# Kernel tuning notes

Measured on AMD Instinct MI355X. Metric: run time of the kernel, lower is better.

Reference implementation:

```python
import jax, jax.numpy as jnp
import numpy as np

D_MODEL = 2048
NUM_HEADS = 16
HEAD_DIM = D_MODEL // NUM_HEADS  # 128


def setup_inputs() -> dict:
    key = jax.random.key(0)
    ks = jax.random.split(key, 11)
    B, S = 2, 2048
    s = 0.02
    return {
        "q": jax.random.normal(ks[0], (B, S, D_MODEL), jnp.float32),
        "k": jax.random.normal(ks[1], (B, S, D_MODEL), jnp.float32),
        "v": jax.random.normal(ks[2], (B, S, D_MODEL), jnp.float32),
        "Wq": jax.random.normal(ks[3], (D_MODEL, D_MODEL), jnp.float32) * s,
        "bq": jnp.zeros((D_MODEL,), jnp.float32),
        "Wk": jax.random.normal(ks[4], (D_MODEL, HEAD_DIM), jnp.float32) * s,
        "bk": jnp.zeros((HEAD_DIM,), jnp.float32),
        "Wv": jax.random.normal(ks[5], (D_MODEL, HEAD_DIM), jnp.float32) * s,
        "bv": jnp.zeros((HEAD_DIM,), jnp.float32),
        "Wo": jax.random.normal(ks[6], (D_MODEL, D_MODEL), jnp.float32) * s,
        "bo": jnp.zeros((D_MODEL,), jnp.float32),
    }


def reference(q, k, v, Wq, bq, Wk, bk, Wv, bv, Wo, bo):
    B, Sq, _ = q.shape
    Skv = k.shape[1]
    # Query projection -> per-head queries [B, H, Sq, Dh]
    qh = (q @ Wq + bq).reshape(B, Sq, NUM_HEADS, HEAD_DIM).transpose(0, 2, 1, 3)
    # Shared single-head K/V projections [B, Skv, Dh]
    kh = k @ Wk + bk
    vh = v @ Wv + bv
    scale = 1.0 / jnp.sqrt(jnp.asarray(HEAD_DIM, qh.dtype))
    # MQA: broadcast shared K over heads without materializing per-head copies
    scores = jnp.einsum("bhqd,bkd->bhqk", qh, kh) * scale  # [B, H, Sq, Skv]
    attn = jax.nn.softmax(scores, axis=-1)
    out = jnp.einsum("bhqk,bkd->bhqd", attn, vh)  # [B, H, Sq, Dh]
    out = out.transpose(0, 2, 1, 3).reshape(B, Sq, D_MODEL)
    return out @ Wo + bo
```

## Files before the change

kernel.cpp:

```cpp
#include <hip/hip_runtime.h>

typedef unsigned short u16;
typedef unsigned int u32;
typedef __bf16 bf16_t;
typedef __attribute__((ext_vector_type(8))) bf16_t bf16x8;
typedef __attribute__((ext_vector_type(4))) float f32x4;

__device__ inline u16 f2bf(float f) {
    union { float f; u32 u; } v; v.f = f;
    u32 u = v.u;
    u32 r = (u + 0x7fffu + ((u >> 16) & 1u)) >> 16;
    return (u16)r;
}

__device__ inline void async_cp16(const void* g, void* l) {
    __builtin_amdgcn_global_load_lds((const __attribute__((address_space(1))) void*)g,
                                     (__attribute__((address_space(3))) void*)l, 16, 0, 0);
}

__global__ __launch_bounds__(256) void cvt3(const float* __restrict__ a,
                                            const float* __restrict__ b,
                                            const float* __restrict__ c,
                                            u16* __restrict__ oa, u16* __restrict__ ob,
                                            u16* __restrict__ oc) {
    int z = blockIdx.y;
    const float* in = z == 0 ? a : (z == 1 ? b : c);
    u16* out = z == 0 ? oa : (z == 1 ? ob : oc);
    int i = (blockIdx.x * 256 + threadIdx.x) * 4;
    float4 f = *(const float4*)(in + i);
    ushort4 o;
    o.x = f2bf(f.x); o.y = f2bf(f.y); o.z = f2bf(f.z); o.w = f2bf(f.w);
    *(ushort4*)(out + i) = o;
}

__global__ __launch_bounds__(256) void transpose2(const float* __restrict__ W0,
                                                  u16* __restrict__ T0,
                                                  const float* __restrict__ W1,
                                                  u16* __restrict__ T1,
                                                  int K, int N) {
    const float* W = blockIdx.z == 0 ? W0 : W1;
    u16* WT = blockIdx.z == 0 ? T0 : T1;
    __shared__ float tile[32][33];
    int tr0 = blockIdx.x * 32;
    int tc0 = blockIdx.y * 32;
    int t = threadIdx.x;
    for (int i = 0; i < 4; i++) {
        int idx = t + i * 256; int r = idx >> 5, c = idx & 31;
        tile[r][c] = W[(size_t)(tr0 + r) * N + tc0 + c];
    }
    __syncthreads();
    for (int i = 0; i < 4; i++) {
        int idx = t + i * 256; int r = idx >> 5, c = idx & 31;
        WT[(size_t)(tc0 + r) * K + tr0 + c] = f2bf(tile[c][r]);
    }
}

template <typename OUT_T>
__global__ __launch_bounds__(256) void gemm_bt(const u16* __restrict__ A,
                                               const u16* __restrict__ BT,
                                               const float* __restrict__ bias,
                                               OUT_T* __restrict__ C,
                                               int M, int N, int K, int ldout) {
    __shared__ u16 sA[128 * 32];
    __shared__ u16 sB[128 * 32];
    int t = threadIdx.x, lane = t & 63, wv = t >> 6;
    int quad = lane >> 4, c16 = lane & 15;
    int bm = blockIdx.x * 128, bn = blockIdx.y * 128;
    int wm = (wv & 1) * 64, wn = (wv >> 1) * 64;
    f32x4 acc[4][4] = {};

    int srow = wv * 32 + (lane >> 2);
    int scol = (lane & 3) * 8;
    const u16* Ag = A + (size_t)(bm + srow) * K + scol;
    const u16* Bg = BT + (size_t)(bn + srow) * K + scol;
    u16* sAd = &sA[(wv * 32) * 32];
    u16* sBd = &sB[(wv * 32) * 32];

    for (int k0 = 0; k0 < K; k0 += 32) {
        __syncthreads();
        async_cp16(Ag + k0, sAd);
        async_cp16(Ag + (size_t)16 * K + k0, sAd + 16 * 32);
        async_cp16(Bg + k0, sBd);
        async_cp16(Bg + (size_t)16 * K + k0, sBd + 16 * 32);
        __syncthreads();
        bf16x8 af[4], bfr[4];
        for (int mi = 0; mi < 4; mi++)
            af[mi] = *(const bf16x8*)&sA[(wm + mi * 16 + c16) * 32 + quad * 8];
        for (int ni = 0; ni < 4; ni++)
            bfr[ni] = *(const bf16x8*)&sB[(wn + ni * 16 + c16) * 32 + quad * 8];
        for (int mi = 0; mi < 4; mi++)
            for (int ni = 0; ni < 4; ni++)
                acc[mi][ni] = __builtin_amdgcn_mfma_f32_16x16x32_bf16(
                    af[mi], bfr[ni], acc[mi][ni], 0, 0, 0);
    }

    for (int mi = 0; mi < 4; mi++) {
        for (int ni = 0; ni < 4; ni++) {
            int col = bn + wn + ni * 16 + c16;
            float bv = bias[col];
            for (int p = 0; p < 4; p++) {
                int row = bm + wm + mi * 16 + quad * 4 + p;
                float v = acc[mi][ni][p] + bv;
                size_t off = (size_t)row * ldout + col;
                if constexpr (__is_same(OUT_T, u16)) C[off] = f2bf(v);
                else C[off] = v;
            }
        }
    }
}

__global__ __launch_bounds__(256) void gemm_kv_sk(const u16* __restrict__ kbf,
                                                  const u16* __restrict__ vbf,
                                                  const u16* __restrict__ WkT,
                                                  const u16* __restrict__ WvT,
                                                  float* __restrict__ kacc,
                                                  float* __restrict__ vacc,
                                                  int K, int KS) {
    bool isv = blockIdx.y == 1;
    const u16* A = isv ? vbf : kbf;
    const u16* BT = isv ? WvT : WkT;
    float* aco = isv ? vacc : kacc;
    __shared__ u16 sA[128 * 32];
    __shared__ u16 sB[128 * 32];
    int t = threadIdx.x, lane = t & 63, wv = t >> 6;
    int quad = lane >> 4, c16 = lane & 15;
    int bm = blockIdx.x * 128;
    int wm = (wv & 1) * 64, wn = (wv >> 1) * 64;
    f32x4 acc[4][4] = {};

    int srow = wv * 32 + (lane >> 2);
    int scol = (lane & 3) * 8;
    const u16* Ag = A + (size_t)(bm + srow) * K + scol;
    const u16* Bg = BT + (size_t)srow * K + scol;
    u16* sAd = &sA[(wv * 32) * 32];
    u16* sBd = &sB[(wv * 32) * 32];

    int kbeg = blockIdx.z * KS;
    for (int k0 = kbeg; k0 < kbeg + KS; k0 += 32) {
        __syncthreads();
        async_cp16(Ag + k0, sAd);
        async_cp16(Ag + (size_t)16 * K + k0, sAd + 16 * 32);
        async_cp16(Bg + k0, sBd);
        async_cp16(Bg + (size_t)16 * K + k0, sBd + 16 * 32);
        __syncthreads();
        bf16x8 af[4], bfr[4];
        for (int mi = 0; mi < 4; mi++)
            af[mi] = *(const bf16x8*)&sA[(wm + mi * 16 + c16) * 32 + quad * 8];
        for (int ni = 0; ni < 4; ni++)
            bfr[ni] = *(const bf16x8*)&sB[(wn + ni * 16 + c16) * 32 + quad * 8];
        for (int mi = 0; mi < 4; mi++)
            for (int ni = 0; ni < 4; ni++)
                acc[mi][ni] = __builtin_amdgcn_mfma_f32_16x16x32_bf16(
                    af[mi], bfr[ni], acc[mi][ni], 0, 0, 0);
    }

    for (int mi = 0; mi < 4; mi++)
        for (int ni = 0; ni < 4; ni++) {
            int col = wn + ni * 16 + c16;
            for (int p = 0; p < 4; p++) {
                int row = bm + wm + mi * 16 + quad * 4 + p;
                atomicAdd(&aco[(size_t)row * 128 + col], acc[mi][ni][p]);
            }
        }
}

__global__ __launch_bounds__(256) void cvt_kv(const float* __restrict__ kacc,
                                              const float* __restrict__ vacc,
                                              const float* __restrict__ bk,
                                              const float* __restrict__ bv,
                                              u16* __restrict__ khb,
                                              u16* __restrict__ vhT,
                                              int M) {
    int t = threadIdx.x;
    int tr0 = blockIdx.x * 32;
    int tc0 = blockIdx.y * 32;
    if (blockIdx.z == 0) {
        for (int i = 0; i < 4; i++) {
            int idx = t + i * 256; int r = idx >> 5, c = idx & 31;
            khb[(size_t)(tr0 + r) * 128 + tc0 + c] =
                f2bf(kacc[(size_t)(tr0 + r) * 128 + tc0 + c] + bk[tc0 + c]);
        }
    } else {
        __shared__ float tile[32][33];
        for (int i = 0; i < 4; i++) {
            int idx = t + i * 256; int r = idx >> 5, c = idx & 31;
            tile[r][c] = vacc[(size_t)(tr0 + r) * 128 + tc0 + c] + bv[tc0 + c];
        }
        __syncthreads();
        for (int i = 0; i < 4; i++) {
            int idx = t + i * 256; int r = idx >> 5, c = idx & 31;
            vhT[(size_t)(tc0 + r) * M + tr0 + c] = f2bf(tile[c][r]);
        }
    }
}

__global__ __launch_bounds__(256, 2) void mqa_attn(const u16* __restrict__ qh,
                                                   const u16* __restrict__ kh,
                                                   const u16* __restrict__ vhT,
                                                   u16* __restrict__ outp,
                                                   int S) {
    constexpr float CEXP = 0.08838834764831845f * 1.4426950408889634f;
    __shared__ u16 smem[40960];
    u16* sK0 = smem;
    u16* sV0 = smem + 16384;
    u16* sP  = smem + 32768;

    int t = threadIdx.x, lane = t & 63, wv = t >> 6;
    int quad = lane >> 4, c16 = lane & 15;
    int rx = c16 & 7;
    int b = blockIdx.z, h = blockIdx.y;
    int q0w = blockIdx.x * 128 + wv * 32;
    int BS = b * S;

    bf16x8 aq[2][4];
    for (int mi = 0; mi < 2; mi++) {
        const u16* qp = qh + (size_t)(BS + q0w + mi * 16 + c16) * 2048 + h * 128 + quad * 8;
        for (int c = 0; c < 4; c++) aq[mi][c] = *(const bf16x8*)(qp + c * 32);
    }

    f32x4 out[2][8] = {};
    f32x4 lsumv[2] = {};
    u16* sPw = sP + wv * 2048;

    int ksub = lane >> 4, kch = lane & 15;
    int klx = (wv * 4 + ksub) & 7;
    const u16* kgb = kh + (size_t)(BS + wv * 4 + ksub) * 128 + ((kch ^ klx) * 8);
    int vsub = lane >> 3, vch = lane & 7;
    int vlx = vsub & 7;
    const u16* vgb = vhT + (size_t)(wv * 8 + vsub) * 4096 + BS + ((vch ^ vlx) * 8);

    u16* kb0 = sK0 + (wv * 4) * 128;
    u16* vb0 = sV0 + (wv * 8) * 64;

    auto STAGE = [&](int kv0, int d) {
        u16* kb = kb0 + d * 8192;
        u16* vb = vb0 + d * 8192;
        for (int p = 0; p < 4; p++)
            async_cp16(kgb + (size_t)(kv0 + p * 16) * 128, kb + p * 2048);
        for (int p = 0; p < 4; p++)
            async_cp16(vgb + (size_t)(p * 32) * 4096 + kv0, vb + p * 2048);
    };

    const int NT = S >> 6;
    STAGE(0, 0);
    __syncthreads();

    for (int tt = 0; tt < NT; tt++) {
        int cur = tt & 1;
        if (tt + 1 < NT) STAGE((tt + 1) * 64, cur ^ 1);
        const u16* sKc = sK0 + cur * 8192;
        const u16* sVc = sV0 + cur * 8192;

        for (int ni = 0; ni < 4; ni++) {
            f32x4 sc[2] = {};
            const u16* kr = sKc + (ni * 16 + c16) * 128;
            for (int c = 0; c < 4; c++) {
                bf16x8 bk = *(const bf16x8*)(kr + ((c * 4 + quad) ^ rx) * 8);
                sc[0] = __builtin_amdgcn_mfma_f32_16x16x32_bf16(bk, aq[0][c], sc[0], 0, 0, 0);
                sc[1] = __builtin_amdgcn_mfma_f32_16x16x32_bf16(bk, aq[1][c], sc[1], 0, 0, 0);
            }
            for (int mi = 0; mi < 2; mi++) {
                u32 eu[4];
                f32x4 et;
                for (int p = 0; p < 4; p++) {
                    float e = __builtin_amdgcn_exp2f(sc[mi][p] * CEXP);
                    union { float f; u32 u; } cv; cv.f = e;
                    eu[p] = cv.u;
                    cv.u &= 0xffff0000u;
                    et[p] = cv.f;
                }
                lsumv[mi] += et;
                u32 pk0 = __builtin_amdgcn_perm(eu[1], eu[0], 0x07060302u);
                u32 pk1 = __builtin_amdgcn_perm(eu[3], eu[2], 0x07060302u);
                *(uint2*)&sPw[(mi * 16 + c16) * 64 +
                              (((ni * 2 + (quad >> 1)) ^ rx) * 8) + (quad & 1) * 4] =
                    make_uint2(pk0, pk1);
            }
        }
        asm volatile("s_waitcnt lgkmcnt(0)" ::: "memory");

        for (int ks = 0; ks < 2; ks++) {
            int kchu = ((ks * 4 + quad) ^ rx) * 8;
            bf16x8 ap0 = *(const bf16x8*)&sPw[(0 * 16 + c16) * 64 + kchu];
            bf16x8 ap1 = *(const bf16x8*)&sPw[(1 * 16 + c16) * 64 + kchu];
            for (int ni = 0; ni < 8; ni++) {
                bf16x8 bv = *(const bf16x8*)(sVc + (ni * 16 + c16) * 64 + kchu);
                out[0][ni] = __builtin_amdgcn_mfma_f32_16x16x32_bf16(ap0, bv, out[0][ni], 0, 0, 0);
                out[1][ni] = __builtin_amdgcn_mfma_f32_16x16x32_bf16(ap1, bv, out[1][ni], 0, 0, 0);
            }
        }

        __syncthreads();
    }

    float lp[2];
    for (int mi = 0; mi < 2; mi++) {
        float x = lsumv[mi][0] + lsumv[mi][1] + lsumv[mi][2] + lsumv[mi][3];
        x += __shfl_xor(x, 16, 64);
        x += __shfl_xor(x, 32, 64);
        lp[mi] = x;
    }
    for (int mi = 0; mi < 2; mi++) {
        float inv[4];
        for (int p = 0; p < 4; p++)
            inv[p] = 1.f / __shfl(lp[mi], quad * 4 + p, 64);
        u16* op = outp + (size_t)(BS + q0w + mi * 16 + quad * 4) * 2048 + h * 128;
        for (int ni = 0; ni < 8; ni++)
            for (int p = 0; p < 4; p++)
                op[(size_t)p * 2048 + ni * 16 + c16] = f2bf(out[mi][ni][p] * inv[p]);
    }
}

extern "C" void kernel_launch(void* const* d_in, const int* in_sizes, int n_in,
                              void* d_out, int out_size, void* d_ws, size_t ws_size,
                              hipStream_t stream) {
    const float* q  = (const float*)d_in[0];
    const float* k  = (const float*)d_in[1];
    const float* v  = (const float*)d_in[2];
    const float* Wq = (const float*)d_in[3];
    const float* bq = (const float*)d_in[4];
    const float* Wk = (const float*)d_in[5];
    const float* bk = (const float*)d_in[6];
    const float* Wv = (const float*)d_in[7];
    const float* bv = (const float*)d_in[8];
    const float* Wo = (const float*)d_in[9];
    const float* bo = (const float*)d_in[10];
    float* out = (float*)d_out;

    const int S = 2048, D = 2048, Dh = 128, M = 4096;
    const int QKV = M * D;
    const int WDD = D * D;
    const int WDH = D * Dh;
    const int MDh = M * Dh;

    u16* ws   = (u16*)d_ws;
    u16* q_bf = ws;
    u16* k_bf = q_bf + QKV;
    u16* v_bf = k_bf + QKV;
    u16* WqT  = v_bf + QKV;
    u16* WoT  = WqT + WDD;
    u16* WkT  = WoT + WDD;
    u16* WvT  = WkT + WDH;
    u16* qhb  = WvT + WDH;
    u16* khb  = qhb + QKV;
    u16* vhTb = khb + MDh;
    u16* aout = vhTb + MDh;
    float* kacc = (float*)(aout + QKV);
    float* vacc = kacc + MDh;

    hipMemsetAsync(kacc, 0, (size_t)2 * MDh * sizeof(float), stream);

    cvt3<<<dim3(QKV / 1024, 3), 256, 0, stream>>>(q, k, v, q_bf, k_bf, v_bf);
    transpose2<<<dim3(64, 64, 2), 256, 0, stream>>>(Wq, WqT, Wo, WoT, D, D);
    transpose2<<<dim3(64, 4, 2), 256, 0, stream>>>(Wk, WkT, Wv, WvT, D, Dh);

    gemm_bt<u16><<<dim3(32, 16), 256, 0, stream>>>(q_bf, WqT, bq, qhb, M, D, D, D);
    gemm_kv_sk<<<dim3(32, 2, 4), 256, 0, stream>>>(k_bf, v_bf, WkT, WvT, kacc, vacc, D, 512);
    cvt_kv<<<dim3(128, 4, 2), 256, 0, stream>>>(kacc, vacc, bk, bv, khb, vhTb, M);

    mqa_attn<<<dim3(16, 16, 2), 256, 0, stream>>>(qhb, khb, vhTb, aout, S);

    gemm_bt<float><<<dim3(32, 16), 256, 0, stream>>>(aout, WoT, bo, out, M, D, D, D);
}
```

Baseline: 387.2 us.

## Rewrite projection GEMMs with triple-buffered async LDS pipeline and 256x128 tiles

Replaces the 128x128, single-buffered bf16 GEMM used for the Q and output projections with a 512-thread kernel computing 256x128 tiles over a K step of 64. It triple-buffers the global-to-LDS async copies, waiting with explicit vmcnt counts, and XOR-swizzles LDS columns to avoid bank conflicts. Block IDs are remapped for L2 locality and MFMA sections are wrapped in setprio. The aim is to hide global load latency and cut per-k-step barrier overhead, at the cost of much more LDS per block (144KB) and fewer resident blocks.

After: 366.2 us. -5.4%, faster.

```diff
diff --git a/kernel.cpp b/kernel.cpp
--- a/kernel.cpp
+++ b/kernel.cpp
@@ -56,50 +56,86 @@
 }
 
 template <typename OUT_T>
-__global__ __launch_bounds__(256) void gemm_bt(const u16* __restrict__ A,
-                                               const u16* __restrict__ BT,
-                                               const float* __restrict__ bias,
-                                               OUT_T* __restrict__ C,
-                                               int M, int N, int K, int ldout) {
-    __shared__ u16 sA[128 * 32];
-    __shared__ u16 sB[128 * 32];
+__global__ __launch_bounds__(512, 2) void gemm_bt2(const u16* __restrict__ A,
+                                                   const u16* __restrict__ BT,
+                                                   const float* __restrict__ bias,
+                                                   OUT_T* __restrict__ C,
+                                                   int M, int N, int K, int ldout) {
+    __shared__ u16 smem[3 * 24576];
     int t = threadIdx.x, lane = t & 63, wv = t >> 6;
     int quad = lane >> 4, c16 = lane & 15;
-    int bm = blockIdx.x * 128, bn = blockIdx.y * 128;
-    int wm = (wv & 1) * 64, wn = (wv >> 1) * 64;
+    int rx = c16 & 7;
+    int wr = wv >> 1, wc = wv & 1;
+
+    int nwg = gridDim.x;
+    int cpx = nwg >> 3;
+    int bid = blockIdx.x;
+    int swz = (bid & 7) * cpx + (bid >> 3);
+    int Mt = M >> 8;
+    int bm = (swz % Mt) << 8;
+    int bn = (swz / Mt) << 7;
+
     f32x4 acc[4][4] = {};
 
-    int srow = wv * 32 + (lane >> 2);
-    int scol = (lane & 3) * 8;
+    int srow = wv * 8 + (lane >> 3);
+    int scol = ((lane & 7) ^ (lane >> 3)) * 8;
     const u16* Ag = A + (size_t)(bm + srow) * K + scol;
     const u16* Bg = BT + (size_t)(bn + srow) * K + scol;
-    u16* sAd = &sA[(wv * 32) * 32];
-    u16* sBd = &sB[(wv * 32) * 32];
-
-    for (int k0 = 0; k0 < K; k0 += 32) {
-        __syncthreads();
-        async_cp16(Ag + k0, sAd);
-        async_cp16(Ag + (size_t)16 * K + k0, sAd + 16 * 32);
-        async_cp16(Bg + k0, sBd);
-        async_cp16(Bg + (size_t)16 * K + k0, sBd + 16 * 32);
-        __syncthreads();
-        bf16x8 af[4], bfr[4];
-        for (int mi = 0; mi < 4; mi++)
-            af[mi] = *(const bf16x8*)&sA[(wm + mi * 16 + c16) * 32 + quad * 8];
-        for (int ni = 0; ni < 4; ni++)
-            bfr[ni] = *(const bf16x8*)&sB[(wn + ni * 16 + c16) * 32 + quad * 8];
-        for (int mi = 0; mi < 4; mi++)
-            for (int ni = 0; ni < 4; ni++)
-                acc[mi][ni] = __builtin_amdgcn_mfma_f32_16x16x32_bf16(
-                    af[mi], bfr[ni], acc[mi][ni], 0, 0, 0);
+
+    auto STAGE = [&](int kt, int d) {
+        u16* base = smem + d * 24576;
+        u16* ad = base + (size_t)(wv * 8) * 64;
+        u16* bd = base + 16384 + (size_t)(wv * 8) * 64;
+        const u16* ag = Ag + (size_t)kt * 64;
+        const u16* bg = Bg + (size_t)kt * 64;
+        for (int p = 0; p < 4; p++)
+            async_cp16(ag + (size_t)(p * 64) * K, ad + p * 4096);
+        for (int p = 0; p < 2; p++)
+            async_cp16(bg + (size_t)(p * 64) * K, bd + p * 4096);
+    };
+
+    const int NT = K >> 6;
+    STAGE(0, 0);
+    STAGE(1, 1);
+
+    for (int tt = 0; tt < NT; tt++) {
+        if (tt + 1 < NT) asm volatile("s_waitcnt vmcnt(6)" ::: "memory");
+        else             asm volatile("s_waitcnt vmcnt(0)" ::: "memory");
+        __builtin_amdgcn_s_barrier();
+        if (tt + 2 < NT) STAGE(tt + 2, (tt + 2) % 3);
+
+        const u16* sA = smem + (tt % 3) * 24576;
+        const u16* sB = sA + 16384;
+
+        for (int rh = 0; rh < 2; rh++) {
+            bf16x8 af[2][2];
+            for (int mi = 0; mi < 2; mi++)
+                for (int kk = 0; kk < 2; kk++)
+                    af[mi][kk] = *(const bf16x8*)&sA[(wr * 64 + rh * 32 + mi * 16 + c16) * 64 +
+                                                     (((kk * 4 + quad) ^ rx) * 8)];
+            for (int ch = 0; ch < 2; ch++) {
+                bf16x8 bf[2][2];
+                for (int ni = 0; ni < 2; ni++)
+                    for (int kk = 0; kk < 2; kk++)
+                        bf[ni][kk] = *(const bf16x8*)&sB[(wc * 64 + ch * 32 + ni * 16 + c16) * 64 +
+                                                         (((kk * 4 + quad) ^ rx) * 8)];
+                __builtin_amdgcn_s_setprio(1);
+                for (int kk = 0; kk < 2; kk++)
+                    for (int mi = 0; mi < 2; mi++)
+                        for (int ni = 0; ni < 2; ni++)
+                            acc[rh * 2 + mi][ch * 2 + ni] = __builtin_amdgcn_mfma_f32_16x16x32_bf16(
+                                af[mi][kk], bf[ni][kk], acc[rh * 2 + mi][ch * 2 + ni], 0, 0, 0);
+                __builtin_amdgcn_s_setprio(0);
+            }
+        }
     }
 
     for (int mi = 0; mi < 4; mi++) {
         for (int ni = 0; ni < 4; ni++) {
-            int col = bn + wn + ni * 16 + c16;
+            int col = bn + wc * 64 + ni * 16 + c16;
             float bv = bias[col];
             for (int p = 0; p < 4; p++) {
-                int row = bm + wm + mi * 16 + quad * 4 + p;
+                int row = bm + wr * 64 + mi * 16 + quad * 4 + p;
                 float v = acc[mi][ni][p] + bv;
                 size_t off = (size_t)row * ldout + col;
                 if constexpr (__is_same(OUT_T, u16)) C[off] = f2bf(v);
@@ -354,11 +390,11 @@
     transpose2<<<dim3(64, 64, 2), 256, 0, stream>>>(Wq, WqT, Wo, WoT, D, D);
     transpose2<<<dim3(64, 4, 2), 256, 0, stream>>>(Wk, WkT, Wv, WvT, D, Dh);
 
-    gemm_bt<u16><<<dim3(32, 16), 256, 0, stream>>>(q_bf, WqT, bq, qhb, M, D, D, D);
+    gemm_bt2<u16><<<dim3(256), 512, 0, stream>>>(q_bf, WqT, bq, qhb, M, D, D, D);
     gemm_kv_sk<<<dim3(32, 2, 4), 256, 0, stream>>>(k_bf, v_bf, WkT, WvT, kacc, vacc, D, 512);
     cvt_kv<<<dim3(128, 4, 2), 256, 0, stream>>>(kacc, vacc, bk, bv, khb, vhTb, M);
 
     mqa_attn<<<dim3(16, 16, 2), 256, 0, stream>>>(qhb, khb, vhTb, aout, S);
 
-    gemm_bt<float><<<dim3(32, 16), 256, 0, stream>>>(aout, WoT, bo, out, M, D, D, D);
-}
+    gemm_bt2<float><<<dim3(256), 512, 0, stream>>>(aout, WoT, bo, out, M, D, D, D);
+}
```
